# Optimization experiments

Hardware: AMD Instinct MI355X
Metric: run time of the kernel (lower is better)

Reference implementation:

```python
import jax, jax.numpy as jnp
import numpy as np

U, I, B = 6000, 3072, 3000
EMB, HEADS, BATCH = 64, 8, 4096
EPS = 1e-8


def _bipartite(rng, r, c, deg):
    m = np.zeros((r, c), np.float32)
    idx = rng.integers(0, c, (r, deg))
    m[np.arange(r)[:, None], idx] = 1.0
    return m


def _rownorm(g):
    return g / (g.sum(1, keepdims=True) + EPS)


def _laplace(g):
    rs = np.sqrt(g.sum(1)) + EPS
    cs = np.sqrt(g.sum(0)) + EPS
    return (g / rs[:, None]) / cs[None, :]


def _xavier(k, shape):
    fan = shape[0] + shape[-1] if len(shape) > 1 else shape[0]
    return jax.random.normal(k, shape, jnp.float32) * np.float32(np.sqrt(2.0 / fan))


def setup_inputs() -> dict:
    rng = np.random.default_rng(0)
    ub = _bipartite(rng, U, B, 10)
    ui = _bipartite(rng, U, I, 20)
    bi = _bipartite(rng, B, I, 15)
    A_i = _rownorm(ui.T @ ui)          # [I,I]
    B_i = _rownorm(bi.T @ bi)          # [I,I]
    ub_norm = _rownorm(ub)
    bu_norm = (ub / (ub.sum(0, keepdims=True) + EPS)).T
    ui_norm = _rownorm(ui)
    iu_norm = (ui / (ui.sum(0, keepdims=True) + EPS)).T
    bi_norm = _rownorm(bi)
    ib_norm = (bi / (bi.sum(0, keepdims=True) + EPS)).T
    ub_graph = _laplace(np.block([[np.eye(U, dtype=np.float32), ub_norm], [bu_norm, np.eye(B, dtype=np.float32)]]))
    ui_graph = _laplace(np.block([[np.eye(U, dtype=np.float32), ui_norm], [iu_norm, np.eye(I, dtype=np.float32)]]))
    ks = jax.random.split(jax.random.key(0), 16)
    inp = {
        'users_feature': _xavier(ks[0], (U, EMB)),
        'items_feature': _xavier(ks[1], (I, EMB)),
        'bundles_feature': _xavier(ks[2], (B, EMB)),
        'Wq': _xavier(ks[3], (EMB, EMB)), 'Wk': _xavier(ks[4], (EMB, EMB)),
        'Wv': _xavier(ks[5], (EMB, EMB)), 'Wo': _xavier(ks[6], (EMB, EMB)),
        'W_ub': _xavier(ks[7], (EMB, EMB)), 'b_ub': jnp.zeros((EMB,), jnp.float32),
        'W_ui': _xavier(ks[8], (EMB, EMB)), 'b_ui': jnp.zeros((EMB,), jnp.float32),
        'att_b_w': _xavier(ks[9], (EMB,)), 'att_i_w': _xavier(ks[10], (EMB,)),
        'p1_W': _xavier(ks[11], (9 * EMB, 8)), 'p1_b': jnp.zeros((8,), jnp.float32),
        'p2_W': _xavier(ks[12], (8, 1)), 'p2_b': jnp.zeros((1,), jnp.float32),
        'A_i': jnp.asarray(A_i), 'B_i': jnp.asarray(B_i),
        'bi_avg': jnp.asarray(bi_norm), 'ui_avg': jnp.asarray(ui_norm),
        'ub_avg': jnp.asarray(ub_norm), 'ib_avg': jnp.asarray(ib_norm),
        'ub_graph': jnp.asarray(ub_graph), 'ui_graph': jnp.asarray(ui_graph),
        'users': jax.random.randint(ks[13], (BATCH,), 0, U),
        'bundles': jax.random.randint(ks[14], (BATCH,), 0, B),
    }
    return inp


def _l2norm(x):
    return x / jnp.maximum(jnp.linalg.norm(x, axis=1, keepdims=True), 1e-12)


def _mhatt(x, Wq, Wk, Wv, Wo):
    n, d = x.shape
    dh = d // HEADS
    q = (x @ Wq).reshape(n, HEADS, dh)
    k = (x @ Wk).reshape(n, HEADS, dh)
    v = (x @ Wv).reshape(n, HEADS, dh)
    a = jax.nn.softmax(jnp.einsum('nhd,mhd->hnm', q, k) / np.float32(np.sqrt(dh)), axis=-1)
    return jnp.einsum('hnm,mhd->nhd', a, v).reshape(n, d) @ Wo


def _att2(x, w):  # x: [N, 2, D], softmax-weighted fusion over the stack axis
    a = jax.nn.softmax(jnp.einsum('ntd,d->nt', x, w), axis=1)
    return jnp.einsum('nt,ntd->nd', a, x)


def reference(users_feature, items_feature, bundles_feature, Wq, Wk, Wv, Wo,
              W_ub, b_ub, W_ui, b_ui, att_b_w, att_i_w,
              p1_W, p1_b, p2_W, p2_b,
              A_i, B_i, bi_avg, ui_avg, ub_avg, ib_avg, ub_graph, ui_graph,
              users, bundles):
    relu = jax.nn.relu
    # Intention
    items0 = relu(A_i @ items_feature) + relu(B_i @ items_feature) + items_feature
    items = _mhatt(items0, Wq, Wk, Wv, Wo)
    bundles_f = relu(bi_avg @ items) + bundles_feature
    users_f = relu(ui_avg @ items) + relu(ub_avg @ bundles_f) + users_feature
    # NPPT (layers = 1)
    f_ub0 = jnp.concatenate([users_f, bundles_f], 0)   # [U+B, E]
    f_ui0 = jnp.concatenate([users_f, items], 0)       # [U+I, E]
    f_ub = relu((ub_graph @ f_ub0) @ W_ub + b_ub)
    f_ui = relu((ui_graph @ f_ui0) @ W_ui + b_ui)
    u1, i1 = f_ui0[:U], f_ui0[U:]
    b1 = _l2norm(relu(bi_avg @ i1))
    ub_fused = _att2(jnp.stack([f_ub0, jnp.concatenate([u1, b1], 0)], 1), att_b_w)
    feat_ub = jnp.concatenate([f_ub, ub_fused], 1)     # [U+B, 2E]
    u2, b2 = f_ub0[:U], f_ub0[U:]
    i2 = _l2norm(relu(ib_avg @ b2))
    ui_fused = _att2(jnp.stack([f_ui0, jnp.concatenate([u2, i2], 0)], 1), att_i_w)
    feat_ui = jnp.concatenate([f_ui, ui_fused], 1)     # computed as in original (unused by ub output)
    all_ub = jnp.concatenate([f_ub0, _l2norm(feat_ub)], 1)  # [U+B, 3E]
    uA, bB = all_ub[:U], all_ub[U:]
    ue = uA[users]
    be = bB[bundles]
    new_emb = jnp.concatenate([ue * be, be, ue], 1)    # [BATCH, 9E]
    return relu(new_emb @ p1_W + p1_b) @ p2_W + p2_b   # [BATCH, 1]
```

## Files before the change

kernel.cpp:

```cpp
#include <hip/hip_runtime.h>
#include <math.h>

typedef float f32x4 __attribute__((ext_vector_type(4)));

__device__ __forceinline__ float wsum64(float v) {
#pragma unroll
  for (int d = 1; d < 64; d <<= 1) v += __shfl_xor(v, d, 64);
  return v;
}

__device__ __forceinline__ float spseg(const float* __restrict__ Arow, int K,
                                       const float* __restrict__ X,
                                       int lane, int wave,
                                       uint2* __restrict__ L)
{
  float acc0 = 0.f, acc1 = 0.f;
  const int nch = (K + 255) >> 8;
  for (int c = wave; c < nch; c += 4) {
    const int k = (c << 8) + lane * 4;
    f32x4 a = {0.f, 0.f, 0.f, 0.f};
    if (k + 4 <= K) {
      a = *(const f32x4*)(Arow + k);
    } else {
#pragma unroll
      for (int j = 0; j < 4; ++j)
        if (k + j < K) a[j] = Arow[k + j];
    }
    const int n0 = (a[0] != 0.f), n1 = (a[1] != 0.f);
    const int n2 = (a[2] != 0.f), n3 = (a[3] != 0.f);
    const int cnt = n0 + n1 + n2 + n3;
    if (__ballot(cnt != 0) == 0ULL) continue;
    int inc = cnt;
#pragma unroll
    for (int d = 1; d < 64; d <<= 1) {
      int t = __shfl_up(inc, d, 64);
      if (lane >= d) inc += t;
    }
    const int total = __shfl(inc, 63, 64);
    int p = inc - cnt;
    if (n0) { L[p] = make_uint2(k,     __float_as_uint(a[0])); p++; }
    if (n1) { L[p] = make_uint2(k + 1, __float_as_uint(a[1])); p++; }
    if (n2) { L[p] = make_uint2(k + 2, __float_as_uint(a[2])); p++; }
    if (n3) { L[p] = make_uint2(k + 3, __float_as_uint(a[3])); p++; }
    asm volatile("s_waitcnt lgkmcnt(0)" ::: "memory");
    int e = 0;
    for (; e + 4 <= total; e += 4) {
      uint2 E0 = L[e], E1 = L[e + 1], E2 = L[e + 2], E3 = L[e + 3];
      float x0 = X[(E0.x << 6) | lane];
      float x1 = X[(E1.x << 6) | lane];
      float x2 = X[(E2.x << 6) | lane];
      float x3 = X[(E3.x << 6) | lane];
      acc0 = fmaf(__uint_as_float(E0.y), x0, acc0);
      acc1 = fmaf(__uint_as_float(E1.y), x1, acc1);
      acc0 = fmaf(__uint_as_float(E2.y), x2, acc0);
      acc1 = fmaf(__uint_as_float(E3.y), x3, acc1);
    }
    for (; e < total; ++e) {
      uint2 E = L[e];
      acc0 = fmaf(__uint_as_float(E.y), X[(E.x << 6) | lane], acc0);
    }
  }
  return acc0 + acc1;
}

__global__ __launch_bounds__(256) void spmm_items0(const float* __restrict__ Ai,
                                                   const float* __restrict__ Bi,
                                                   const float* __restrict__ itf,
                                                   float* __restrict__ items0)
{
  __shared__ uint2 lists[4][256];
  __shared__ float red[4][2][64];
  const int r = blockIdx.x;
  const int lane = threadIdx.x & 63, wave = threadIdx.x >> 6;
  float sa = spseg(Ai + (size_t)r * 3072, 3072, itf, lane, wave, lists[wave]);
  float sb = spseg(Bi + (size_t)r * 3072, 3072, itf, lane, wave, lists[wave]);
  red[wave][0][lane] = sa;
  red[wave][1][lane] = sb;
  __syncthreads();
  if (threadIdx.x < 64) {
    float a1 = red[0][0][lane] + red[1][0][lane] + red[2][0][lane] + red[3][0][lane];
    float a2 = red[0][1][lane] + red[1][1][lane] + red[2][1][lane] + red[3][1][lane];
    items0[(size_t)r * 64 + lane] =
        fmaxf(a1, 0.f) + fmaxf(a2, 0.f) + itf[(size_t)r * 64 + lane];
  }
}

__global__ __launch_bounds__(256) void spmm_bundle(const float* __restrict__ biA,
                                                   const float* __restrict__ items,
                                                   const float* __restrict__ bfeat,
                                                   float* __restrict__ fub0,
                                                   float* __restrict__ b1)
{
  __shared__ uint2 lists[4][256];
  __shared__ float red[4][64];
  const int r = blockIdx.x;
  const int lane = threadIdx.x & 63, wave = threadIdx.x >> 6;
  float s = spseg(biA + (size_t)r * 3072, 3072, items, lane, wave, lists[wave]);
  red[wave][lane] = s;
  __syncthreads();
  if (threadIdx.x < 64) {
    float acc = red[0][lane] + red[1][lane] + red[2][lane] + red[3][lane];
    float pv = fmaxf(acc, 0.f);
    fub0[(size_t)(6000 + r) * 64 + lane] = pv + bfeat[(size_t)r * 64 + lane];
    float n2 = wsum64(pv * pv);
    b1[(size_t)r * 64 + lane] = pv / fmaxf(sqrtf(n2), 1e-12f);
  }
}

__global__ __launch_bounds__(256) void spmm_users(const float* __restrict__ uiA,
                                                  const float* __restrict__ ubA,
                                                  const float* __restrict__ items,
                                                  const float* __restrict__ bundles_f,
                                                  const float* __restrict__ ufeat,
                                                  float* __restrict__ fub0)
{
  __shared__ uint2 lists[4][256];
  __shared__ float red[4][2][64];
  const int r = blockIdx.x;
  const int lane = threadIdx.x & 63, wave = threadIdx.x >> 6;
  float sa = spseg(uiA + (size_t)r * 3072, 3072, items, lane, wave, lists[wave]);
  float sb = spseg(ubA + (size_t)r * 3000, 3000, bundles_f, lane, wave, lists[wave]);
  red[wave][0][lane] = sa;
  red[wave][1][lane] = sb;
  __syncthreads();
  if (threadIdx.x < 64) {
    float a1 = red[0][0][lane] + red[1][0][lane] + red[2][0][lane] + red[3][0][lane];
    float a2 = red[0][1][lane] + red[1][1][lane] + red[2][1][lane] + red[3][1][lane];
    fub0[(size_t)r * 64 + lane] =
        fmaxf(a1, 0.f) + fmaxf(a2, 0.f) + ufeat[(size_t)r * 64 + lane];
  }
}

__global__ __launch_bounds__(256) void spmm_ubg(const float* __restrict__ ubg,
                                                const float* __restrict__ f0W,
                                                const float* __restrict__ b_ub,
                                                const float* __restrict__ fub0,
                                                const float* __restrict__ b1,
                                                const float* __restrict__ att_w,
                                                float* __restrict__ all_ub)
{
  __shared__ uint2 lists[4][256];
  __shared__ float red[4][64];
  const int r = blockIdx.x;
  const int lane = threadIdx.x & 63, wave = threadIdx.x >> 6;
  float s = spseg(ubg + (size_t)r * 9000, 9000, f0W, lane, wave, lists[wave]);
  red[wave][lane] = s;
  __syncthreads();
  if (threadIdx.x < 64) {
    float acc = red[0][lane] + red[1][lane] + red[2][lane] + red[3][lane];
    float fu = fmaxf(acc + b_ub[lane], 0.f);
    float x0 = fub0[(size_t)r * 64 + lane];
    float x1 = (r < 6000) ? x0 : b1[(size_t)(r - 6000) * 64 + lane];
    float wv = att_w[lane];
    float s0 = wsum64(x0 * wv);
    float s1 = wsum64(x1 * wv);
    float m = fmaxf(s0, s1);
    float e0 = __expf(s0 - m), e1 = __expf(s1 - m);
    float fused = (e0 * x0 + e1 * x1) / (e0 + e1);
    float n2 = wsum64(fu * fu + fused * fused);
    float inv = 1.f / fmaxf(sqrtf(n2), 1e-12f);
    float* row = &all_ub[(size_t)r * 192];
    row[lane]       = x0;
    row[64 + lane]  = fu * inv;
    row[128 + lane] = fused * inv;
  }
}

__global__ __launch_bounds__(256) void rowgemm64(const float* __restrict__ A,
                                                 const float* __restrict__ W,
                                                 float* __restrict__ C, int M)
{
  __shared__ float Ws[64][64];
  __shared__ float As[4][64];
  for (int i = threadIdx.x; i < 1024; i += 256)
    ((f32x4*)&Ws[0][0])[i] = ((const f32x4*)W)[i];
  const int wave = threadIdx.x >> 6, lane = threadIdx.x & 63;
  const int r = blockIdx.x * 4 + wave;
  const bool valid = r < M;
  As[wave][lane] = valid ? A[(size_t)r * 64 + lane] : 0.f;
  __syncthreads();
  float acc = 0.f;
#pragma unroll
  for (int k = 0; k < 64; ++k)
    acc = fmaf(As[wave][k], Ws[k][lane], acc);
  if (valid) C[(size_t)r * 64 + lane] = acc;
}

__global__ __launch_bounds__(256) void rowgemm64_qkv(const float* __restrict__ A,
                                                     const float* __restrict__ Wq,
                                                     const float* __restrict__ Wk,
                                                     const float* __restrict__ Wv,
                                                     float* __restrict__ qb,
                                                     float* __restrict__ kb,
                                                     float* __restrict__ vb)
{
  const float* W = (blockIdx.y == 0) ? Wq : (blockIdx.y == 1) ? Wk : Wv;
  float* C = (blockIdx.y == 0) ? qb : (blockIdx.y == 1) ? kb : vb;
  __shared__ float Ws[64][64];
  __shared__ float As[4][64];
  for (int i = threadIdx.x; i < 1024; i += 256)
    ((f32x4*)&Ws[0][0])[i] = ((const f32x4*)W)[i];
  const int wave = threadIdx.x >> 6, lane = threadIdx.x & 63;
  const int r = blockIdx.x * 4 + wave;
  As[wave][lane] = A[(size_t)r * 64 + lane];
  __syncthreads();
  float acc = 0.f;
#pragma unroll
  for (int k = 0; k < 64; ++k)
    acc = fmaf(As[wave][k], Ws[k][lane], acc);
  C[(size_t)r * 64 + lane] = acc;
}

__global__ __launch_bounds__(256) void attn_kernel(const float* __restrict__ q,
                                                   const float* __restrict__ k,
                                                   const float* __restrict__ v,
                                                   float* __restrict__ o)
{
  __shared__ float Ks[256][8];
  __shared__ float Vs[256][8];
  const int h = blockIdx.y;
  const int tid = threadIdx.x;
  const int qi = tid >> 3, p = tid & 7;
  const int n = blockIdx.x * 32 + qi;

  float qr[8];
#pragma unroll
  for (int j = 0; j < 8; ++j) qr[j] = q[n * 64 + h * 8 + j] * 0.3535533905932738f;

  float mx = -1e30f, sum = 0.f, acc[8] = {};

  for (int m0 = 0; m0 < 3072; m0 += 256) {
    __syncthreads();
    {
      const float* kp = &k[(size_t)(m0 + tid) * 64 + h * 8];
      const float* vp = &v[(size_t)(m0 + tid) * 64 + h * 8];
      float4 a0 = *reinterpret_cast<const float4*>(kp);
      float4 a1 = *reinterpret_cast<const float4*>(kp + 4);
      float4 b0 = *reinterpret_cast<const float4*>(vp);
      float4 b1 = *reinterpret_cast<const float4*>(vp + 4);
      *reinterpret_cast<float4*>(&Ks[tid][0]) = a0;
      *reinterpret_cast<float4*>(&Ks[tid][4]) = a1;
      *reinterpret_cast<float4*>(&Vs[tid][0]) = b0;
      *reinterpret_cast<float4*>(&Vs[tid][4]) = b1;
    }
    __syncthreads();
    for (int mm = p; mm < 256; mm += 8) {
      float s = 0.f;
#pragma unroll
      for (int j = 0; j < 8; ++j) s = fmaf(qr[j], Ks[mm][j], s);
      float nm = fmaxf(mx, s);
      float corr = __expf(mx - nm);
      float w = __expf(s - nm);
      sum = sum * corr + w;
#pragma unroll
      for (int j = 0; j < 8; ++j) acc[j] = acc[j] * corr + w * Vs[mm][j];
      mx = nm;
    }
  }
#pragma unroll
  for (int d = 1; d < 8; d <<= 1) {
    float omx = __shfl_xor(mx, d, 64);
    float osum = __shfl_xor(sum, d, 64);
    float nm = fmaxf(mx, omx);
    float c1 = __expf(mx - nm), c2 = __expf(omx - nm);
    float nsum = sum * c1 + osum * c2;
#pragma unroll
    for (int j = 0; j < 8; ++j) {
      float oa = __shfl_xor(acc[j], d, 64);
      acc[j] = acc[j] * c1 + oa * c2;
    }
    mx = nm; sum = nsum;
  }
  if (p == 0) {
    float inv = 1.f / sum;
#pragma unroll
    for (int j = 0; j < 8; ++j) o[n * 64 + h * 8 + j] = acc[j] * inv;
  }
}

__global__ __launch_bounds__(256) void final_mlp(const float* __restrict__ all_ub,
                                                 const int* __restrict__ users,
                                                 const int* __restrict__ bundles,
                                                 const float* __restrict__ p1W,
                                                 const float* __restrict__ p1b,
                                                 const float* __restrict__ p2W,
                                                 const float* __restrict__ p2b,
                                                 float* __restrict__ out)
{
  __shared__ float W[576 * 8];
  for (int i = threadIdx.x; i < 576 * 8; i += 256) W[i] = p1W[i];
  __syncthreads();
  int j = blockIdx.x * 4 + (threadIdx.x >> 6);
  int lane = threadIdx.x & 63;
  const float* ue = &all_ub[(size_t)users[j] * 192];
  const float* be = &all_ub[(size_t)(6000 + bundles[j]) * 192];
  float hacc[8] = {};
#pragma unroll
  for (int db = 0; db < 9; ++db) {
    int d = db * 64 + lane;
    float ne;
    if (d < 192)      ne = ue[d] * be[d];
    else if (d < 384) ne = be[d - 192];
    else              ne = ue[d - 384];
#pragma unroll
    for (int h = 0; h < 8; ++h) hacc[h] = fmaf(ne, W[d * 8 + h], hacc[h]);
  }
#pragma unroll
  for (int d = 1; d < 64; d <<= 1)
#pragma unroll
    for (int h = 0; h < 8; ++h) hacc[h] += __shfl_xor(hacc[h], d, 64);
  if (lane == 0) {
    float o = p2b[0];
#pragma unroll
    for (int h = 0; h < 8; ++h) o += fmaxf(hacc[h] + p1b[h], 0.f) * p2W[h];
    out[j] = o;
  }
}

extern "C" void kernel_launch(void* const* d_in, const int* in_sizes, int n_in,
                              void* d_out, int out_size, void* d_ws, size_t ws_size,
                              hipStream_t stream)
{
  const float* ufeat   = (const float*)d_in[0];
  const float* ifeat   = (const float*)d_in[1];
  const float* bfeat   = (const float*)d_in[2];
  const float* Wq      = (const float*)d_in[3];
  const float* Wk      = (const float*)d_in[4];
  const float* Wv      = (const float*)d_in[5];
  const float* Wo      = (const float*)d_in[6];
  const float* W_ub    = (const float*)d_in[7];
  const float* b_ub    = (const float*)d_in[8];
  const float* att_b_w = (const float*)d_in[11];
  const float* p1W     = (const float*)d_in[13];
  const float* p1b     = (const float*)d_in[14];
  const float* p2W     = (const float*)d_in[15];
  const float* p2b     = (const float*)d_in[16];
  const float* A_i     = (const float*)d_in[17];
  const float* B_i     = (const float*)d_in[18];
  const float* bi_avg  = (const float*)d_in[19];
  const float* ui_avg  = (const float*)d_in[20];
  const float* ub_avg  = (const float*)d_in[21];
  const float* ubg     = (const float*)d_in[23];
  const int* users     = (const int*)d_in[25];
  const int* bundles   = (const int*)d_in[26];

  float* ws = (float*)d_ws;
  float* items0 = ws;  ws += 3072 * 64;
  float* qb     = ws;  ws += 3072 * 64;
  float* kb     = ws;  ws += 3072 * 64;
  float* vb     = ws;  ws += 3072 * 64;
  float* attnb  = ws;  ws += 3072 * 64;
  float* items  = ws;  ws += 3072 * 64;
  float* b1     = ws;  ws += 3000 * 64;
  float* fub0   = ws;  ws += 9000 * 64;
  float* f0W    = ws;  ws += 9000 * 64;
  float* all_ub = ws;  ws += 9000 * 192;

  spmm_items0<<<3072, 256, 0, stream>>>(A_i, B_i, ifeat, items0);

  rowgemm64_qkv<<<dim3(768, 3), 256, 0, stream>>>(items0, Wq, Wk, Wv, qb, kb, vb);
  attn_kernel<<<dim3(96, 8), 256, 0, stream>>>(qb, kb, vb, attnb);
  rowgemm64<<<768, 256, 0, stream>>>(attnb, Wo, items, 3072);

  spmm_bundle<<<3000, 256, 0, stream>>>(bi_avg, items, bfeat, fub0, b1);
  spmm_users<<<6000, 256, 0, stream>>>(ui_avg, ub_avg, items,
                                       fub0 + (size_t)6000 * 64, ufeat, fub0);

  rowgemm64<<<2250, 256, 0, stream>>>(fub0, W_ub, f0W, 9000);

  spmm_ubg<<<9000, 256, 0, stream>>>(ubg, f0W, b_ub, fub0, b1, att_b_w, all_ub);

  final_mlp<<<1024, 256, 0, stream>>>(all_ub, users, bundles, p1W, p1b, p2W, p2b,
                                      (float*)d_out);
}
```

Before: 933.2 us.

## Prefetch sparse chunks, fuse W_ub projection into SpMM, block-wise softmax in attention

The dense-scan sparse routine now loads the next 256-column chunk before processing the current one, so the global load latency of the mostly-zero rows overlaps with compaction and gather. The W_ub projection is folded into the epilogues of the bundle and user SpMM kernels, which removes a separate 9000-row GEMM launch and a re-read of fub0. The attention inner loop computes 32 scores first, then applies a single max/rescale per tile instead of an online rescale per key, which cuts exp calls. The costs are extra registers (32 scores plus a prefetched vector) and a serial 64-step matvec on only one wave per block.

```diff
diff --git a/kernel.cpp b/kernel.cpp
--- a/kernel.cpp
+++ b/kernel.cpp
@@ -7,6 +7,21 @@
 #pragma unroll
   for (int d = 1; d < 64; d <<= 1) v += __shfl_xor(v, d, 64);
   return v;
+}
+
+__device__ __forceinline__ f32x4 ldchunk(const float* __restrict__ Arow, int K,
+                                         int c, int lane)
+{
+  const int k = (c << 8) + lane * 4;
+  f32x4 a = {0.f, 0.f, 0.f, 0.f};
+  if (k + 4 <= K) {
+    a = *(const f32x4*)(Arow + k);
+  } else if (k < K) {
+#pragma unroll
+    for (int j = 0; j < 4; ++j)
+      if (k + j < K) a[j] = Arow[k + j];
+  }
+  return a;
 }
 
 __device__ __forceinline__ float spseg(const float* __restrict__ Arow, int K,
@@ -16,49 +31,51 @@
 {
   float acc0 = 0.f, acc1 = 0.f;
   const int nch = (K + 255) >> 8;
-  for (int c = wave; c < nch; c += 4) {
+  int c = wave;
+  if (c >= nch) return 0.f;
+  f32x4 a = ldchunk(Arow, K, c, lane);
+  while (c < nch) {
+    const int cn = c + 4;
+    f32x4 an = {0.f, 0.f, 0.f, 0.f};
+    if (cn < nch) an = ldchunk(Arow, K, cn, lane);
+
     const int k = (c << 8) + lane * 4;
-    f32x4 a = {0.f, 0.f, 0.f, 0.f};
-    if (k + 4 <= K) {
-      a = *(const f32x4*)(Arow + k);
-    } else {
-#pragma unroll
-      for (int j = 0; j < 4; ++j)
-        if (k + j < K) a[j] = Arow[k + j];
-    }
     const int n0 = (a[0] != 0.f), n1 = (a[1] != 0.f);
     const int n2 = (a[2] != 0.f), n3 = (a[3] != 0.f);
     const int cnt = n0 + n1 + n2 + n3;
-    if (__ballot(cnt != 0) == 0ULL) continue;
-    int inc = cnt;
-#pragma unroll
-    for (int d = 1; d < 64; d <<= 1) {
-      int t = __shfl_up(inc, d, 64);
-      if (lane >= d) inc += t;
-    }
-    const int total = __shfl(inc, 63, 64);
-    int p = inc - cnt;
-    if (n0) { L[p] = make_uint2(k,     __float_as_uint(a[0])); p++; }
-    if (n1) { L[p] = make_uint2(k + 1, __float_as_uint(a[1])); p++; }
-    if (n2) { L[p] = make_uint2(k + 2, __float_as_uint(a[2])); p++; }
-    if (n3) { L[p] = make_uint2(k + 3, __float_as_uint(a[3])); p++; }
-    asm volatile("s_waitcnt lgkmcnt(0)" ::: "memory");
-    int e = 0;
-    for (; e + 4 <= total; e += 4) {
-      uint2 E0 = L[e], E1 = L[e + 1], E2 = L[e + 2], E3 = L[e + 3];
-      float x0 = X[(E0.x << 6) | lane];
-      float x1 = X[(E1.x << 6) | lane];
-      float x2 = X[(E2.x << 6) | lane];
-      float x3 = X[(E3.x << 6) | lane];
-      acc0 = fmaf(__uint_as_float(E0.y), x0, acc0);
-      acc1 = fmaf(__uint_as_float(E1.y), x1, acc1);
-      acc0 = fmaf(__uint_as_float(E2.y), x2, acc0);
-      acc1 = fmaf(__uint_as_float(E3.y), x3, acc1);
-    }
-    for (; e < total; ++e) {
-      uint2 E = L[e];
-      acc0 = fmaf(__uint_as_float(E.y), X[(E.x << 6) | lane], acc0);
-    }
+    if (__ballot(cnt != 0) != 0ULL) {
+      int inc = cnt;
+#pragma unroll
+      for (int d = 1; d < 64; d <<= 1) {
+        int t = __shfl_up(inc, d, 64);
+        if (lane >= d) inc += t;
+      }
+      const int total = __shfl(inc, 63, 64);
+      int p = inc - cnt;
+      if (n0) { L[p] = make_uint2(k,     __float_as_uint(a[0])); p++; }
+      if (n1) { L[p] = make_uint2(k + 1, __float_as_uint(a[1])); p++; }
+      if (n2) { L[p] = make_uint2(k + 2, __float_as_uint(a[2])); p++; }
+      if (n3) { L[p] = make_uint2(k + 3, __float_as_uint(a[3])); p++; }
+      asm volatile("s_waitcnt lgkmcnt(0)" ::: "memory");
+      int e = 0;
+      for (; e + 4 <= total; e += 4) {
+        uint2 E0 = L[e], E1 = L[e + 1], E2 = L[e + 2], E3 = L[e + 3];
+        float x0 = X[(E0.x << 6) | lane];
+        float x1 = X[(E1.x << 6) | lane];
+        float x2 = X[(E2.x << 6) | lane];
+        float x3 = X[(E3.x << 6) | lane];
+        acc0 = fmaf(__uint_as_float(E0.y), x0, acc0);
+        acc1 = fmaf(__uint_as_float(E1.y), x1, acc1);
+        acc0 = fmaf(__uint_as_float(E2.y), x2, acc0);
+        acc1 = fmaf(__uint_as_float(E3.y), x3, acc1);
+      }
+      for (; e < total; ++e) {
+        uint2 E = L[e];
+        acc0 = fmaf(__uint_as_float(E.y), X[(E.x << 6) | lane], acc0);
+      }
+    }
+    a = an;
+    c = cn;
   }
   return acc0 + acc1;
 }
@@ -88,11 +105,14 @@
 __global__ __launch_bounds__(256) void spmm_bundle(const float* __restrict__ biA,
                                                    const float* __restrict__ items,
                                                    const float* __restrict__ bfeat,
+                                                   const float* __restrict__ W_ub,
                                                    float* __restrict__ fub0,
-                                                   float* __restrict__ b1)
+                                                   float* __restrict__ b1,
+                                                   float* __restrict__ f0W)
 {
   __shared__ uint2 lists[4][256];
   __shared__ float red[4][64];
+  __shared__ float rowsh[64];
   const int r = blockIdx.x;
   const int lane = threadIdx.x & 63, wave = threadIdx.x >> 6;
   float s = spseg(biA + (size_t)r * 3072, 3072, items, lane, wave, lists[wave]);
@@ -101,9 +121,19 @@
   if (threadIdx.x < 64) {
     float acc = red[0][lane] + red[1][lane] + red[2][lane] + red[3][lane];
     float pv = fmaxf(acc, 0.f);
-    fub0[(size_t)(6000 + r) * 64 + lane] = pv + bfeat[(size_t)r * 64 + lane];
+    float fv = pv + bfeat[(size_t)r * 64 + lane];
+    fub0[(size_t)(6000 + r) * 64 + lane] = fv;
     float n2 = wsum64(pv * pv);
     b1[(size_t)r * 64 + lane] = pv / fmaxf(sqrtf(n2), 1e-12f);
+    rowsh[lane] = fv;
+    asm volatile("s_waitcnt lgkmcnt(0)" ::: "memory");
+    float w0 = 0.f, w1 = 0.f;
+#pragma unroll
+    for (int k = 0; k < 64; k += 2) {
+      w0 = fmaf(rowsh[k],     W_ub[k * 64 + lane],       w0);
+      w1 = fmaf(rowsh[k + 1], W_ub[(k + 1) * 64 + lane], w1);
+    }
+    f0W[(size_t)(6000 + r) * 64 + lane] = w0 + w1;
   }
 }
 
@@ -112,10 +142,13 @@
                                                   const float* __restrict__ items,
                                                   const float* __restrict__ bundles_f,
                                                   const float* __restrict__ ufeat,
-                                                  float* __restrict__ fub0)
+                                                  const float* __restrict__ W_ub,
+                                                  float* __restrict__ fub0,
+                                                  float* __restrict__ f0W)
 {
   __shared__ uint2 lists[4][256];
   __shared__ float red[4][2][64];
+  __shared__ float rowsh[64];
   const int r = blockIdx.x;
   const int lane = threadIdx.x & 63, wave = threadIdx.x >> 6;
   float sa = spseg(uiA + (size_t)r * 3072, 3072, items, lane, wave, lists[wave]);
@@ -126,8 +159,17 @@
   if (threadIdx.x < 64) {
     float a1 = red[0][0][lane] + red[1][0][lane] + red[2][0][lane] + red[3][0][lane];
     float a2 = red[0][1][lane] + red[1][1][lane] + red[2][1][lane] + red[3][1][lane];
-    fub0[(size_t)r * 64 + lane] =
-        fmaxf(a1, 0.f) + fmaxf(a2, 0.f) + ufeat[(size_t)r * 64 + lane];
+    float fv = fmaxf(a1, 0.f) + fmaxf(a2, 0.f) + ufeat[(size_t)r * 64 + lane];
+    fub0[(size_t)r * 64 + lane] = fv;
+    rowsh[lane] = fv;
+    asm volatile("s_waitcnt lgkmcnt(0)" ::: "memory");
+    float w0 = 0.f, w1 = 0.f;
+#pragma unroll
+    for (int k = 0; k < 64; k += 2) {
+      w0 = fmaf(rowsh[k],     W_ub[k * 64 + lane],       w0);
+      w1 = fmaf(rowsh[k + 1], W_ub[(k + 1) * 64 + lane], w1);
+    }
+    f0W[(size_t)r * 64 + lane] = w0 + w1;
   }
 }
 
@@ -244,18 +286,33 @@
       *reinterpret_cast<float4*>(&Vs[tid][4]) = b1;
     }
     __syncthreads();
-    for (int mm = p; mm < 256; mm += 8) {
-      float s = 0.f;
-#pragma unroll
-      for (int j = 0; j < 8; ++j) s = fmaf(qr[j], Ks[mm][j], s);
-      float nm = fmaxf(mx, s);
-      float corr = __expf(mx - nm);
-      float w = __expf(s - nm);
-      sum = sum * corr + w;
-#pragma unroll
-      for (int j = 0; j < 8; ++j) acc[j] = acc[j] * corr + w * Vs[mm][j];
-      mx = nm;
-    }
+
+    float s[32];
+#pragma unroll
+    for (int i = 0; i < 32; ++i) {
+      const int mm = p + i * 8;
+      float t = 0.f;
+#pragma unroll
+      for (int j = 0; j < 8; ++j) t = fmaf(qr[j], Ks[mm][j], t);
+      s[i] = t;
+    }
+    float lmax = s[0];
+#pragma unroll
+    for (int i = 1; i < 32; ++i) lmax = fmaxf(lmax, s[i]);
+    const float nm = fmaxf(mx, lmax);
+    const float corr = __expf(mx - nm);
+    sum *= corr;
+#pragma unroll
+    for (int j = 0; j < 8; ++j) acc[j] *= corr;
+#pragma unroll
+    for (int i = 0; i < 32; ++i) {
+      const int mm = p + i * 8;
+      const float w = __expf(s[i] - nm);
+      sum += w;
+#pragma unroll
+      for (int j = 0; j < 8; ++j) acc[j] = fmaf(w, Vs[mm][j], acc[j]);
+    }
+    mx = nm;
   }
 #pragma unroll
   for (int d = 1; d < 8; d <<= 1) {
@@ -362,11 +419,10 @@
   attn_kernel<<<dim3(96, 8), 256, 0, stream>>>(qb, kb, vb, attnb);
   rowgemm64<<<768, 256, 0, stream>>>(attnb, Wo, items, 3072);
 
-  spmm_bundle<<<3000, 256, 0, stream>>>(bi_avg, items, bfeat, fub0, b1);
+  spmm_bundle<<<3000, 256, 0, stream>>>(bi_avg, items, bfeat, W_ub, fub0, b1, f0W);
   spmm_users<<<6000, 256, 0, stream>>>(ui_avg, ub_avg, items,
-                                       fub0 + (size_t)6000 * 64, ufeat, fub0);
-
-  rowgemm64<<<2250, 256, 0, stream>>>(fub0, W_ub, f0W, 9000);
+                                       fub0 + (size_t)6000 * 64, ufeat, W_ub,
+                                       fub0, f0W);
 
   spmm_ubg<<<9000, 256, 0, stream>>>(ubg, f0W, b_ub, fub0, b1, att_b_w, all_ub);
 
```

Result: no change. 915.1 us (-1.9%).
